# Kernel tuning notes

Measured on AMD Instinct MI355X. Metric: run time of the kernel, lower is better.

## Reference

```python
import jax, jax.numpy as jnp
import numpy as np

BRANCH = 8
LEVELS = 7
N = (BRANCH ** LEVELS - 1) // (BRANCH - 1)  # 299593 nodes, complete 8-ary tree
VOCAB, IN_DIM, MEM = 50000, 300, 150


def _tree_structure():
    parent = np.empty(N, np.int32)
    parent[0] = N  # sentinel: root scatters into dropped segment N
    idx = np.arange(1, N)
    parent[1:] = (idx - 1) // BRANCH
    depth = np.empty(N, np.int32)
    start = 0
    for d in range(LEVELS):
        cnt = BRANCH ** d
        depth[start:start + cnt] = d
        start += cnt
    return jnp.asarray(parent), jnp.asarray(depth)


def setup_inputs() -> dict:
    key = jax.random.key(0)
    ks = jax.random.split(key, 20)
    parent, depth = _tree_structure()
    inp = {
        'tokens': jax.random.randint(ks[0], (N,), 0, VOCAB, dtype=jnp.int32),
        'parent': parent,
        'depth': depth,
        'max_depth': LEVELS,
        'emb': jax.random.normal(ks[1], (VOCAB, IN_DIM), jnp.float32) * 0.1,
    }
    names_x = ['Wix', 'Wfx', 'Wox', 'Wux']
    names_h = ['Wih', 'Wfh', 'Woh', 'Wuh']
    sx = 1.0 / np.sqrt(IN_DIM)
    sh = 1.0 / np.sqrt(MEM)
    for j, (nx, nh) in enumerate(zip(names_x, names_h)):
        inp[nx] = jax.random.normal(ks[2 + 4 * j], (MEM, IN_DIM), jnp.float32) * sx
        inp['b' + nx[1:]] = jax.random.normal(ks[3 + 4 * j], (MEM,), jnp.float32) * sx
        inp[nh] = jax.random.normal(ks[4 + 4 * j], (MEM, MEM), jnp.float32) * sh
        inp['b' + nh[1:]] = jax.random.normal(ks[5 + 4 * j], (MEM,), jnp.float32) * sh
    return inp


def reference(tokens, parent, depth, max_depth, emb,
              Wix, bix, Wih, bih, Wfx, bfx, Wfh, bfh,
              Wox, box, Woh, boh, Wux, bux, Wuh, buh):
    n = tokens.shape[0]
    x = emb[tokens]  # [N, in_dim]
    # precompute all input-side gate projections once (batched GEMMs)
    ix_x = x @ Wix.T + bix
    fx_x = x @ Wfx.T + bfx
    ox_x = x @ Wox.T + box
    ux_x = x @ Wux.T + bux
    # parent index safe for gathering (root's sentinel -> 0; its row is masked out)
    gparent = jnp.where(parent >= n, 0, parent)

    h = jnp.zeros((n, MEM), x.dtype)
    c = jnp.zeros((n, MEM), x.dtype)

    # level-synchronous bottom-up sweep (loop over tree depth, not data)
    for d in range(max_depth - 1, -1, -1):
        # per-child forget gate: sigmoid(fh(h_child) + fx(x_parent)) * c_child
        f = jax.nn.sigmoid(h @ Wfh.T + bfh + fx_x[gparent])
        fc_sum = jax.ops.segment_sum(f * c, parent, num_segments=n + 1)[:n]
        h_sum = jax.ops.segment_sum(h, parent, num_segments=n + 1)[:n]
        i = jax.nn.sigmoid(ix_x + h_sum @ Wih.T + bih)
        o = jax.nn.sigmoid(ox_x + h_sum @ Woh.T + boh)
        u = jnp.tanh(ux_x + h_sum @ Wuh.T + buh)
        c_new = i * u + fc_sum
        h_new = o * jnp.tanh(c_new)
        mask = (depth == d)[:, None]
        c = jnp.where(mask, c_new, c)
        h = jnp.where(mask, h_new, h)
    # original returns concatenated cell states (post-order); here indexed by node id
    return c
```

## Files before the change

### kernel.cpp

```cpp
#include <hip/hip_runtime.h>


#define MEMD  150
#define IND   300
#define NINT  37449
#define VOCAB 50000
#define GROW  608
#define FSTR  152

typedef short bf16x8 __attribute__((ext_vector_type(8)));
typedef float f32x16 __attribute__((ext_vector_type(16)));
#define ZERO16 {0,0,0,0,0,0,0,0,0,0,0,0,0,0,0,0}

#define GALL_OFF 0ul
#define HSB_OFF  60800000ul
#define FCS_OFF  72200000ul
#define BPX_OFF  94980000ul
#define BPH_OFF  95380000ul

__device__ __forceinline__ float b2f(unsigned short u) {
    union { unsigned int i; float f; } v; v.i = ((unsigned int)u) << 16; return v.f;
}
__device__ __forceinline__ unsigned short f2b(float f) {
    union { float f; unsigned int i; } v; v.f = f;
    unsigned int x = v.i;
    x += 0x7fffu + ((x >> 16) & 1u);
    return (unsigned short)(x >> 16);
}
__device__ __forceinline__ float sigm(float x) {
    return __builtin_amdgcn_rcpf(1.0f + __expf(-x));
}
__device__ __forceinline__ float tanh_fast(float x) {
    float e = __expf(2.0f * x);
    return 1.0f - 2.0f * __builtin_amdgcn_rcpf(e + 1.0f);
}

__global__ void pack_w(const float* __restrict__ Wix, const float* __restrict__ Wox,
                       const float* __restrict__ Wux, const float* __restrict__ Wfx,
                       const float* __restrict__ Wih, const float* __restrict__ Woh,
                       const float* __restrict__ Wuh, const float* __restrict__ Wfh,
                       unsigned short* __restrict__ bpx, unsigned short* __restrict__ bph)
{
    const int total_x = 4 * 5 * 19 * 512;
    const int total_h = 4 * 5 * 10 * 512;
    for (int i = blockIdx.x * blockDim.x + threadIdx.x; i < total_x + total_h;
         i += gridDim.x * blockDim.x) {
        if (i < total_x) {
            int e = i & 7, lane = (i >> 3) & 63, rest = i >> 9;
            int ks = rest % 19; rest /= 19;
            int nt = rest % 5;  int g = rest / 5;
            int col = nt * 32 + (lane & 31);
            int k = ks * 16 + ((lane >> 5) << 3) + e;
            const float* W = (g == 0) ? Wix : (g == 1) ? Wox : (g == 2) ? Wux : Wfx;
            bpx[i] = f2b((col < MEMD && k < IND) ? W[col * IND + k] : 0.f);
        } else {
            int j = i - total_x;
            int e = j & 7, lane = (j >> 3) & 63, rest = j >> 9;
            int ks = rest % 10; rest /= 10;
            int nt = rest % 5;  int g = rest / 5;
            int col = nt * 32 + (lane & 31);
            int k = ks * 16 + ((lane >> 5) << 3) + e;
            const float* W = (g == 0) ? Wih : (g == 1) ? Woh : (g == 2) ? Wuh : Wfh;
            bph[j] = f2b((col < MEMD && k < MEMD) ? W[col * MEMD + k] : 0.f);
        }
    }
}

__global__ __launch_bounds__(640, 2)
void vocab_gemm(const float* __restrict__ emb,
                const float* __restrict__ bix, const float* __restrict__ bih,
                const float* __restrict__ box_, const float* __restrict__ boh,
                const float* __restrict__ bux, const float* __restrict__ buh,
                const float* __restrict__ bfx, const float* __restrict__ bfh,
                const unsigned short* __restrict__ bpx_u,
                unsigned short* __restrict__ gall)
{
    __shared__ __align__(16) char sm0[40960];
    const int tid = threadIdx.x, lane = tid & 63, w = tid >> 6;
    const int hi = lane >> 5, ln31 = lane & 31;
    const int tile0 = blockIdx.x * 64;
    const int rowsValid = min(64, VOCAB - tile0);
    const int mt = (w >= 5) ? 1 : 0, nt = w - mt * 5;

    for (int i = tid; i < 64 * 40; i += 640) {
        int r = i / 40, q = i % 40;
        int rr = (r < rowsValid) ? r : 0;
        const float* er = emb + (long)(tile0 + rr) * IND;
        float4 v0 = {0.f,0.f,0.f,0.f}, v1 = {0.f,0.f,0.f,0.f};
        if (q < 38) v0 = *(const float4*)(er + q * 8);
        if (q < 37) v1 = *(const float4*)(er + q * 8 + 4);
        bf16x8 p;
        p[0]=(short)f2b(v0.x); p[1]=(short)f2b(v0.y); p[2]=(short)f2b(v0.z); p[3]=(short)f2b(v0.w);
        p[4]=(short)f2b(v1.x); p[5]=(short)f2b(v1.y); p[6]=(short)f2b(v1.z); p[7]=(short)f2b(v1.w);
        *(bf16x8*)(sm0 + r * 640 + ((q * 16) ^ ((r & 7) << 4))) = p;
    }
    __syncthreads();

    const bf16x8* BX = (const bf16x8*)bpx_u;
    const int row = mt * 32 + ln31;
    const int col = nt * 32 + ln31;
    const bool colv = col < MEMD;
    const int cc = colv ? col : 0;
    const float* b1[4] = {bix, box_, bux, bfx};
    const float* b2[4] = {bih, boh, buh, bfh};

    for (int g = 0; g < 4; ++g) {
        f32x16 acc = ZERO16;
        bf16x8 aC = *(const bf16x8*)(sm0 + row * 640 + ((0) ^ ((row & 7) << 4)));
        bf16x8 bC = BX[((g * 5 + nt) * 19 + 0) * 64 + lane];
        #pragma unroll
        for (int ks = 0; ks < 19; ++ks) {
            bf16x8 aN, bN;
            if (ks < 18) {
                aN = *(const bf16x8*)(sm0 + row * 640 + (((ks + 1) * 32 + hi * 16) ^ ((row & 7) << 4)));
                bN = BX[((g * 5 + nt) * 19 + ks + 1) * 64 + lane];
            }
            if (ks == 0) aC = *(const bf16x8*)(sm0 + row * 640 + ((hi * 16) ^ ((row & 7) << 4)));
            acc = __builtin_amdgcn_mfma_f32_32x32x16_bf16(aC, bC, acc, 0, 0, 0);
            aC = aN; bC = bN;
        }
        float bias = colv ? (b1[g][cc] + b2[g][cc]) : 0.f;
        #pragma unroll
        for (int r = 0; r < 16; ++r) {
            int rloc = mt * 32 + (r & 3) + 8 * (r >> 2) + 4 * hi;
            if (rloc < rowsValid && colv)
                gall[(long)(tile0 + rloc) * GROW + col * 4 + g] = f2b(acc[r] + bias);
        }
    }
}

template<bool INTERNAL>
__global__ __launch_bounds__(320, INTERNAL ? 2 : 4)
void level_k(const int* __restrict__ tokens,
             const unsigned short* __restrict__ gall,
             const unsigned short* __restrict__ bph_u,
             unsigned short* __restrict__ hsumb, float* __restrict__ fcsum,
             float* __restrict__ c_out, int base, int cnt, int writePar)
{
    __shared__ __align__(16) char sm0[INTERNAL ? 24576 : 12288];
    __shared__ int toksL[32];
    __shared__ int ptokL[4];
    const int tid = threadIdx.x, lane = tid & 63, w = tid >> 6;
    const int hi = lane >> 5, ln31 = lane & 31;
    const int tile0 = blockIdx.x * 32;
    const int nodeBase = base + tile0;
    const int rowsValid = min(32, cnt - tile0);
    const int p0 = (nodeBase - 1) >> 3;
    const int nt = w;

    if (tid < 32) toksL[tid] = tokens[nodeBase + ((tid < rowsValid) ? tid : 0)];
    if (writePar && tid < 4) ptokL[tid] = tokens[p0 + tid];
    if (INTERNAL) {
        for (int i = tid; i < 32 * 20; i += 320) {
            int r = i / 20, q = i % 20;
            bf16x8 v = {0,0,0,0,0,0,0,0};
            if (q < 19)
                v = *(const bf16x8*)(hsumb + (long)(nodeBase + r) * FSTR + q * 8);
            *(bf16x8*)(sm0 + 12288 + r * 384 + ((q * 16) ^ ((r & 7) << 4))) = v;
        }
    }
    __syncthreads();

    const bf16x8* BH = (const bf16x8*)bph_u;
    const int row = ln31;
    const int col = nt * 32 + ln31;
    const bool colv = col < MEMD;
    const int cc = colv ? col : 0;

    f32x16 ai = ZERO16, ao = ZERO16, au = ZERO16;
    if (INTERNAL) {
        const char* hb = sm0 + 12288;
        bf16x8 aC = *(const bf16x8*)(hb + row * 384 + ((hi * 16) ^ ((row & 7) << 4)));
        bf16x8 b0C = BH[((0 * 5 + nt) * 10 + 0) * 64 + lane];
        bf16x8 b1C = BH[((1 * 5 + nt) * 10 + 0) * 64 + lane];
        bf16x8 b2C = BH[((2 * 5 + nt) * 10 + 0) * 64 + lane];
        #pragma unroll
        for (int ks = 0; ks < 10; ++ks) {
            bf16x8 aN, b0N, b1N, b2N;
            if (ks < 9) {
                aN  = *(const bf16x8*)(hb + row * 384 + (((ks + 1) * 32 + hi * 16) ^ ((row & 7) << 4)));
                b0N = BH[((0 * 5 + nt) * 10 + ks + 1) * 64 + lane];
                b1N = BH[((1 * 5 + nt) * 10 + ks + 1) * 64 + lane];
                b2N = BH[((2 * 5 + nt) * 10 + ks + 1) * 64 + lane];
            }
            ai = __builtin_amdgcn_mfma_f32_32x32x16_bf16(aC, b0C, ai, 0, 0, 0);
            ao = __builtin_amdgcn_mfma_f32_32x32x16_bf16(aC, b1C, ao, 0, 0, 0);
            au = __builtin_amdgcn_mfma_f32_32x32x16_bf16(aC, b2C, au, 0, 0, 0);
            aC = aN; b0C = b0N; b1C = b1N; b2C = b2N;
        }
    }

    float cvv[16];
    {
        ushort4 gv[16];
        #pragma unroll
        for (int r = 0; r < 16; ++r) {
            int rloc = (r & 3) + 8 * (r >> 2) + 4 * hi;
            gv[r] = *(const ushort4*)(gall + (long)toksL[rloc] * GROW + cc * 4);
        }
        float hp[4] = {0.f, 0.f, 0.f, 0.f};
        #pragma unroll
        for (int r = 0; r < 16; ++r) {
            int rloc = (r & 3) + 8 * (r >> 2) + 4 * hi;
            bool rv = rloc < rowsValid;
            float fc = 0.f;
            if (INTERNAL) fc = (rv && colv) ? fcsum[(long)(nodeBase + rloc) * FSTR + col] : 0.f;
            float iv = sigm((INTERNAL ? ai[r] : 0.f) + b2f(gv[r].x));
            float ov = sigm((INTERNAL ? ao[r] : 0.f) + b2f(gv[r].y));
            float uv = tanh_fast((INTERNAL ? au[r] : 0.f) + b2f(gv[r].z));
            float cv = iv * uv + fc;
            float h = (rv && colv) ? ov * tanh_fast(cv) : 0.f;
            cvv[r] = (rv && colv) ? cv : 0.f;
            if (rv && colv) c_out[(long)(nodeBase + rloc) * MEMD + col] = cv;
            *(unsigned short*)(sm0 + rloc * 384 + ((col * 2) ^ ((rloc & 7) << 4))) = f2b(h);
            hp[r >> 2] += h;
        }
        if (writePar) {
            #pragma unroll
            for (int o = 0; o < 4; ++o) {
                float s = hp[o] + __shfl_xor(hp[o], 32);
                if (lane < 32 && colv && o * 8 < rowsValid)
                    hsumb[(long)(p0 + o) * FSTR + col] = f2b(s);
            }
        }
    }
    __syncthreads();

    if (writePar) {
        f32x16 ff = ZERO16;
        {
            bf16x8 aC = *(const bf16x8*)(sm0 + row * 384 + ((hi * 16) ^ ((row & 7) << 4)));
            bf16x8 bC = BH[((15 + nt) * 10 + 0) * 64 + lane];
            #pragma unroll
            for (int ks = 0; ks < 10; ++ks) {
                bf16x8 aN, bN;
                if (ks < 9) {
                    aN = *(const bf16x8*)(sm0 + row * 384 + (((ks + 1) * 32 + hi * 16) ^ ((row & 7) << 4)));
                    bN = BH[((15 + nt) * 10 + ks + 1) * 64 + lane];
                }
                ff = __builtin_amdgcn_mfma_f32_32x32x16_bf16(aC, bC, ff, 0, 0, 0);
                aC = aN; bC = bN;
            }
        }
        #pragma unroll
        for (int o = 0; o < 4; ++o) {
            float fx = b2f(gall[(long)ptokL[o] * GROW + cc * 4 + 3]);
            float fp = 0.f;
            #pragma unroll
            for (int q = 0; q < 4; ++q) {
                int r = o * 4 + q;
                fp += sigm(ff[r] + fx) * cvv[r];
            }
            float s = fp + __shfl_xor(fp, 32);
            if (lane < 32 && colv && o * 8 < rowsValid)
                fcsum[(long)(p0 + o) * FSTR + col] = s;
        }
    }
}

extern "C" void kernel_launch(void* const* d_in, const int* in_sizes, int n_in,
                              void* d_out, int out_size, void* d_ws, size_t ws_size,
                              hipStream_t stream) {
    const int*   tokens = (const int*)d_in[0];
    const float* emb = (const float*)d_in[4];
    const float* Wix = (const float*)d_in[5];  const float* bix = (const float*)d_in[6];
    const float* Wih = (const float*)d_in[7];  const float* bih = (const float*)d_in[8];
    const float* Wfx = (const float*)d_in[9];  const float* bfx = (const float*)d_in[10];
    const float* Wfh = (const float*)d_in[11]; const float* bfh = (const float*)d_in[12];
    const float* Wox = (const float*)d_in[13]; const float* box_ = (const float*)d_in[14];
    const float* Woh = (const float*)d_in[15]; const float* boh = (const float*)d_in[16];
    const float* Wux = (const float*)d_in[17]; const float* bux = (const float*)d_in[18];
    const float* Wuh = (const float*)d_in[19]; const float* buh = (const float*)d_in[20];
    float* c_out = (float*)d_out;
    char* ws = (char*)d_ws;

    unsigned short* gall  = (unsigned short*)(ws + GALL_OFF);
    unsigned short* hsumb = (unsigned short*)(ws + HSB_OFF);
    float*          fcs   = (float*)(ws + FCS_OFF);
    unsigned short* bpx   = (unsigned short*)(ws + BPX_OFF);
    unsigned short* bph   = (unsigned short*)(ws + BPH_OFF);

    pack_w<<<128, 512, 0, stream>>>(Wix, Wox, Wux, Wfx, Wih, Woh, Wuh, Wfh, bpx, bph);
    vocab_gemm<<<(VOCAB + 63) / 64, 640, 0, stream>>>(
        emb, bix, bih, box_, boh, bux, buh, bfx, bfh, bpx, gall);

    static const int bases[7] = {0, 1, 9, 73, 585, 4681, 37449};
    static const int cnts[7]  = {1, 8, 64, 512, 4096, 32768, 262144};

    level_k<false><<<cnts[6] / 32, 320, 0, stream>>>(
        tokens, gall, bph, hsumb, fcs, c_out, bases[6], cnts[6], 1);
    for (int d = 5; d >= 0; --d) {
        int grid = (cnts[d] + 31) / 32;
        level_k<true><<<grid, 320, 0, stream>>>(
            tokens, gall, bph, hsumb, fcs, c_out, bases[d], cnts[d], (d > 0) ? 1 : 0);
    }
}
```

Before: 297.3 us.

## Fuse top three tree levels into one kernel and store forget sums in bf16

Replaces the three smallest-level launches (64, 8 and 1 nodes) with a single one-block tail kernel that loops over those levels with block barriers, cutting launch overhead on tiny grids. The per-parent forget-sum buffer is stored in bf16 instead of fp32, halving its traffic at some precision cost. The leaf kernel's occupancy hint is raised to 8 and its row-validity checks are removed. The gate-projection gathers are also moved inside the elementwise loop, which lowers register pressure.

```diff
diff --git a/kernel.cpp b/kernel.cpp
--- a/kernel.cpp
+++ b/kernel.cpp
@@ -106,7 +106,7 @@
 
     for (int g = 0; g < 4; ++g) {
         f32x16 acc = ZERO16;
-        bf16x8 aC = *(const bf16x8*)(sm0 + row * 640 + ((0) ^ ((row & 7) << 4)));
+        bf16x8 aC = *(const bf16x8*)(sm0 + row * 640 + ((hi * 16) ^ ((row & 7) << 4)));
         bf16x8 bC = BX[((g * 5 + nt) * 19 + 0) * 64 + lane];
         #pragma unroll
         for (int ks = 0; ks < 19; ++ks) {
@@ -115,7 +115,6 @@
                 aN = *(const bf16x8*)(sm0 + row * 640 + (((ks + 1) * 32 + hi * 16) ^ ((row & 7) << 4)));
                 bN = BX[((g * 5 + nt) * 19 + ks + 1) * 64 + lane];
             }
-            if (ks == 0) aC = *(const bf16x8*)(sm0 + row * 640 + ((hi * 16) ^ ((row & 7) << 4)));
             acc = __builtin_amdgcn_mfma_f32_32x32x16_bf16(aC, bC, acc, 0, 0, 0);
             aC = aN; bC = bN;
         }
@@ -130,11 +129,11 @@
 }
 
 template<bool INTERNAL>
-__global__ __launch_bounds__(320, INTERNAL ? 2 : 4)
+__global__ __launch_bounds__(320, INTERNAL ? 2 : 8)
 void level_k(const int* __restrict__ tokens,
              const unsigned short* __restrict__ gall,
              const unsigned short* __restrict__ bph_u,
-             unsigned short* __restrict__ hsumb, float* __restrict__ fcsum,
+             unsigned short* __restrict__ hsumb, unsigned short* __restrict__ fcsum,
              float* __restrict__ c_out, int base, int cnt, int writePar)
 {
     __shared__ __align__(16) char sm0[INTERNAL ? 24576 : 12288];
@@ -144,7 +143,7 @@
     const int hi = lane >> 5, ln31 = lane & 31;
     const int tile0 = blockIdx.x * 32;
     const int nodeBase = base + tile0;
-    const int rowsValid = min(32, cnt - tile0);
+    const int rowsValid = INTERNAL ? min(32, cnt - tile0) : 32;
     const int p0 = (nodeBase - 1) >> 3;
     const int nt = w;
 
@@ -153,9 +152,10 @@
     if (INTERNAL) {
         for (int i = tid; i < 32 * 20; i += 320) {
             int r = i / 20, q = i % 20;
+            int rr = (r < rowsValid) ? r : 0;
             bf16x8 v = {0,0,0,0,0,0,0,0};
             if (q < 19)
-                v = *(const bf16x8*)(hsumb + (long)(nodeBase + r) * FSTR + q * 8);
+                v = *(const bf16x8*)(hsumb + (long)(nodeBase + rr) * FSTR + q * 8);
             *(bf16x8*)(sm0 + 12288 + r * 384 + ((q * 16) ^ ((r & 7) << 4))) = v;
         }
     }
@@ -192,22 +192,17 @@
 
     float cvv[16];
     {
-        ushort4 gv[16];
-        #pragma unroll
-        for (int r = 0; r < 16; ++r) {
-            int rloc = (r & 3) + 8 * (r >> 2) + 4 * hi;
-            gv[r] = *(const ushort4*)(gall + (long)toksL[rloc] * GROW + cc * 4);
-        }
         float hp[4] = {0.f, 0.f, 0.f, 0.f};
         #pragma unroll
         for (int r = 0; r < 16; ++r) {
             int rloc = (r & 3) + 8 * (r >> 2) + 4 * hi;
-            bool rv = rloc < rowsValid;
+            bool rv = INTERNAL ? (rloc < rowsValid) : true;
+            ushort4 gv = *(const ushort4*)(gall + (long)toksL[rloc] * GROW + cc * 4);
             float fc = 0.f;
-            if (INTERNAL) fc = (rv && colv) ? fcsum[(long)(nodeBase + rloc) * FSTR + col] : 0.f;
-            float iv = sigm((INTERNAL ? ai[r] : 0.f) + b2f(gv[r].x));
-            float ov = sigm((INTERNAL ? ao[r] : 0.f) + b2f(gv[r].y));
-            float uv = tanh_fast((INTERNAL ? au[r] : 0.f) + b2f(gv[r].z));
+            if (INTERNAL) fc = (rv && colv) ? b2f(fcsum[(long)(nodeBase + rloc) * FSTR + col]) : 0.f;
+            float iv = sigm((INTERNAL ? ai[r] : 0.f) + b2f(gv.x));
+            float ov = sigm((INTERNAL ? ao[r] : 0.f) + b2f(gv.y));
+            float uv = tanh_fast((INTERNAL ? au[r] : 0.f) + b2f(gv.z));
             float cv = iv * uv + fc;
             float h = (rv && colv) ? ov * tanh_fast(cv) : 0.f;
             cvv[r] = (rv && colv) ? cv : 0.f;
@@ -219,7 +214,7 @@
             #pragma unroll
             for (int o = 0; o < 4; ++o) {
                 float s = hp[o] + __shfl_xor(hp[o], 32);
-                if (lane < 32 && colv && o * 8 < rowsValid)
+                if (lane < 32 && colv && (INTERNAL ? (o * 8 < rowsValid) : true))
                     hsumb[(long)(p0 + o) * FSTR + col] = f2b(s);
             }
         }
@@ -252,8 +247,116 @@
                 fp += sigm(ff[r] + fx) * cvv[r];
             }
             float s = fp + __shfl_xor(fp, 32);
-            if (lane < 32 && colv && o * 8 < rowsValid)
-                fcsum[(long)(p0 + o) * FSTR + col] = s;
+            if (lane < 32 && colv && (INTERNAL ? (o * 8 < rowsValid) : true))
+                fcsum[(long)(p0 + o) * FSTR + col] = f2b(s);
+        }
+    }
+}
+
+__global__ __launch_bounds__(320, 2)
+void tail_k(const int* __restrict__ tokens,
+            const unsigned short* __restrict__ gall,
+            const unsigned short* __restrict__ bph_u,
+            unsigned short* __restrict__ hsumb, unsigned short* __restrict__ fcsum,
+            float* __restrict__ c_out)
+{
+    __shared__ __align__(16) char sm0[24576];
+    __shared__ int toksL[32];
+    __shared__ int ptokL[4];
+    const int tid = threadIdx.x, lane = tid & 63, w = tid >> 6;
+    const int hi = lane >> 5, ln31 = lane & 31;
+    const int nt = w;
+    const bf16x8* BH = (const bf16x8*)bph_u;
+    const int row = ln31;
+    const int col = nt * 32 + ln31;
+    const bool colv = col < MEMD;
+    const int cc = colv ? col : 0;
+
+    const int basesL[3] = {9, 1, 0};
+    const int cntsL[3]  = {64, 8, 1};
+    const int wpL[3]    = {1, 1, 0};
+
+    for (int li = 0; li < 3; ++li) {
+        for (int t0 = 0; t0 < cntsL[li]; t0 += 32) {
+            const int nodeBase = basesL[li] + t0;
+            const int rowsValid = min(32, cntsL[li] - t0);
+            const int p0 = (nodeBase - 1) >> 3;
+            const int writePar = wpL[li];
+
+            if (tid < 32) toksL[tid] = tokens[nodeBase + ((tid < rowsValid) ? tid : 0)];
+            if (writePar && tid < 4) ptokL[tid] = tokens[p0 + tid];
+            for (int i = tid; i < 32 * 20; i += 320) {
+                int r = i / 20, q = i % 20;
+                int rr = (r < rowsValid) ? r : 0;
+                bf16x8 v = {0,0,0,0,0,0,0,0};
+                if (q < 19)
+                    v = *(const bf16x8*)(hsumb + (long)(nodeBase + rr) * FSTR + q * 8);
+                *(bf16x8*)(sm0 + 12288 + r * 384 + ((q * 16) ^ ((r & 7) << 4))) = v;
+            }
+            __syncthreads();
+
+            f32x16 ai = ZERO16, ao = ZERO16, au = ZERO16;
+            {
+                const char* hb = sm0 + 12288;
+                #pragma unroll
+                for (int ks = 0; ks < 10; ++ks) {
+                    bf16x8 a = *(const bf16x8*)(hb + row * 384 + ((ks * 32 + hi * 16) ^ ((row & 7) << 4)));
+                    ai = __builtin_amdgcn_mfma_f32_32x32x16_bf16(a, BH[((0 * 5 + nt) * 10 + ks) * 64 + lane], ai, 0, 0, 0);
+                    ao = __builtin_amdgcn_mfma_f32_32x32x16_bf16(a, BH[((1 * 5 + nt) * 10 + ks) * 64 + lane], ao, 0, 0, 0);
+                    au = __builtin_amdgcn_mfma_f32_32x32x16_bf16(a, BH[((2 * 5 + nt) * 10 + ks) * 64 + lane], au, 0, 0, 0);
+                }
+            }
+
+            float cvv[16];
+            {
+                float hp[4] = {0.f, 0.f, 0.f, 0.f};
+                #pragma unroll
+                for (int r = 0; r < 16; ++r) {
+                    int rloc = (r & 3) + 8 * (r >> 2) + 4 * hi;
+                    bool rv = rloc < rowsValid;
+                    ushort4 gv = *(const ushort4*)(gall + (long)toksL[rloc] * GROW + cc * 4);
+                    float fc = (rv && colv) ? b2f(fcsum[(long)(nodeBase + rloc) * FSTR + col]) : 0.f;
+                    float iv = sigm(ai[r] + b2f(gv.x));
+                    float ov = sigm(ao[r] + b2f(gv.y));
+                    float uv = tanh_fast(au[r] + b2f(gv.z));
+                    float cv = iv * uv + fc;
+                    float h = (rv && colv) ? ov * tanh_fast(cv) : 0.f;
+                    cvv[r] = (rv && colv) ? cv : 0.f;
+                    if (rv && colv) c_out[(long)(nodeBase + rloc) * MEMD + col] = cv;
+                    *(unsigned short*)(sm0 + rloc * 384 + ((col * 2) ^ ((rloc & 7) << 4))) = f2b(h);
+                    hp[r >> 2] += h;
+                }
+                if (writePar) {
+                    #pragma unroll
+                    for (int o = 0; o < 4; ++o) {
+                        float s = hp[o] + __shfl_xor(hp[o], 32);
+                        if (lane < 32 && colv && o * 8 < rowsValid)
+                            hsumb[(long)(p0 + o) * FSTR + col] = f2b(s);
+                    }
+                }
+            }
+            __syncthreads();
+
+            if (writePar) {
+                f32x16 ff = ZERO16;
+                #pragma unroll
+                for (int ks = 0; ks < 10; ++ks) {
+                    bf16x8 a = *(const bf16x8*)(sm0 + row * 384 + ((ks * 32 + hi * 16) ^ ((row & 7) << 4)));
+                    ff = __builtin_amdgcn_mfma_f32_32x32x16_bf16(a, BH[((15 + nt) * 10 + ks) * 64 + lane], ff, 0, 0, 0);
+                }
+                #pragma unroll
+                for (int o = 0; o < 4; ++o) {
+                    float fx = b2f(gall[(long)ptokL[o] * GROW + cc * 4 + 3]);
+                    float fp = 0.f;
+                    #pragma unroll
+                    for (int q = 0; q < 4; ++q)
+                        fp += sigm(ff[o * 4 + q] + fx) * cvv[o * 4 + q];
+                    float s = fp + __shfl_xor(fp, 32);
+                    if (lane < 32 && colv && o * 8 < rowsValid)
+                        fcsum[(long)(p0 + o) * FSTR + col] = f2b(s);
+                }
+            }
+            __syncthreads();
         }
     }
 }
@@ -276,7 +379,7 @@
 
     unsigned short* gall  = (unsigned short*)(ws + GALL_OFF);
     unsigned short* hsumb = (unsigned short*)(ws + HSB_OFF);
-    float*          fcs   = (float*)(ws + FCS_OFF);
+    unsigned short* fcs   = (unsigned short*)(ws + FCS_OFF);
     unsigned short* bpx   = (unsigned short*)(ws + BPX_OFF);
     unsigned short* bph   = (unsigned short*)(ws + BPH_OFF);
 
@@ -289,9 +392,10 @@
 
     level_k<false><<<cnts[6] / 32, 320, 0, stream>>>(
         tokens, gall, bph, hsumb, fcs, c_out, bases[6], cnts[6], 1);
-    for (int d = 5; d >= 0; --d) {
+    for (int d = 5; d >= 3; --d) {
         int grid = (cnts[d] + 31) / 32;
         level_k<true><<<grid, 320, 0, stream>>>(
-            tokens, gall, bph, hsumb, fcs, c_out, bases[d], cnts[d], (d > 0) ? 1 : 0);
-    }
-}
+            tokens, gall, bph, hsumb, fcs, c_out, bases[d], cnts[d], 1);
+    }
+    tail_k<<<1, 320, 0, stream>>>(tokens, gall, bph, hsumb, fcs, c_out);
+}
```

Measured after the change: 302.9 us. About the same (+1.9%).
